# Optimization experiments

Measured on AMD Instinct MI355X. Metric: run time of the kernel, lower is better.

Reference implementation:

```python
import jax, jax.numpy as jnp
import numpy as np

B, C, H, W = 32, 512, 32, 32
D = C // 8

def setup_inputs() -> dict:
    key = jax.random.key(0)
    ks = jax.random.split(key, 5)
    return {
        "x": jax.random.normal(ks[0], (B, C, H, W), dtype=jnp.float32),
        "w1": jax.random.normal(ks[1], (D, C), dtype=jnp.float32) * (1.0 / np.sqrt(C)),
        "b1": jax.random.normal(ks[2], (D,), dtype=jnp.float32) * 0.01,
        "w2": jax.random.normal(ks[3], (C, C), dtype=jnp.float32) * (1.0 / np.sqrt(C)),
        "b2": jax.random.normal(ks[4], (C,), dtype=jnp.float32) * 0.01,
    }

def reference(x, w1, b1, w2, b2):
    b, c, h, w = x.shape
    n = h * w
    xf = x.reshape(b, c, n)                                   # [B,C,N]
    # 1x1 convs == channel-mixing GEMMs; conv1 is shared for q and k
    qk = jnp.einsum('bcn,dc->bdn', xf, w1) + b1[None, :, None]  # [B,D,N]
    v = jnp.einsum('bcn,oc->bon', xf, w2) + b2[None, :, None]   # [B,C,N]
    q = qk.transpose(0, 2, 1)                                 # [B,N,D]
    attn = jax.nn.softmax(jnp.einsum('bnd,bdm->bnm', q, qk), axis=-1)  # [B,N,N]
    out = jnp.einsum('bnm,bcm->bnc', attn, v)                 # [B,N,C]
    # Faithful quirk: original views [B,N,C] directly as [B,C,H,W] (no transpose)
    return x + out.reshape(b, c, h, w)
```

## Files before the change

### kernel.cpp

```cpp
#include <hip/hip_runtime.h>
#include <hip/hip_bf16.h>
#include <math.h>

#define B_ 32
#define C_ 512
#define N_ 1024
#define D_ 64
#define OPAD 640

typedef __attribute__((ext_vector_type(4))) float f32x4;
typedef __attribute__((ext_vector_type(4))) float float4v;
typedef __attribute__((ext_vector_type(8))) __bf16 bf16x8;

#define MFMA16(a, b, c) __builtin_amdgcn_mfma_f32_16x16x32_bf16((a), (b), (c), 0, 0, 0)

__device__ inline void load_lds16(const void* g, void* l) {
    __builtin_amdgcn_global_load_lds(
        (const __attribute__((address_space(1))) void*)g,
        (__attribute__((address_space(3))) void*)l, 16, 0, 0);
}

__global__ __launch_bounds__(256) void k_transpose_cast(
        const float* __restrict__ x,
        const float* __restrict__ w1, const float* __restrict__ w2,
        __hip_bfloat16* __restrict__ xT, __hip_bfloat16* __restrict__ Wbf) {
    __shared__ float tile[64][68];
    int b = blockIdx.z;
    int n0 = blockIdx.x * 64;
    int c0 = blockIdx.y * 64;
    int t = threadIdx.x;

    int lid = blockIdx.x + 16 * blockIdx.y + 128 * blockIdx.z;
    if (lid < 160) {
        int base = lid * 2048 + t * 8;
        int m = base >> 9, k = base & 511;
        alignas(16) __hip_bfloat16 wtmp[8];
        if (m < D_ + C_) {
            const float* s = (m < D_) ? w1 + (size_t)m * C_ + k
                                      : w2 + (size_t)(m - D_) * C_ + k;
            float4v a = *(const float4v*)s;
            float4v c = *(const float4v*)(s + 4);
            wtmp[0] = __float2bfloat16(a.x); wtmp[1] = __float2bfloat16(a.y);
            wtmp[2] = __float2bfloat16(a.z); wtmp[3] = __float2bfloat16(a.w);
            wtmp[4] = __float2bfloat16(c.x); wtmp[5] = __float2bfloat16(c.y);
            wtmp[6] = __float2bfloat16(c.z); wtmp[7] = __float2bfloat16(c.w);
        } else {
#pragma unroll
            for (int j = 0; j < 8; j++) wtmp[j] = __float2bfloat16(0.0f);
        }
        *(bf16x8*)(Wbf + base) = *(bf16x8*)wtmp;
    }

    const float* xb = x + (size_t)b * (C_ * N_);
#pragma unroll
    for (int i = 0; i < 4; i++) {
        int c = i * 16 + (t >> 4);
        int nc = (t & 15) * 4;
        *(float4v*)&tile[c][nc] =
            *(const float4v*)(xb + (size_t)(c0 + c) * N_ + n0 + nc);
    }
    __syncthreads();
    __hip_bfloat16* xTb = xT + (size_t)b * (N_ * C_);
#pragma unroll
    for (int i = 0; i < 2; i++) {
        int n = i * 32 + (t >> 3);
        int cs = (t & 7) * 8;
        alignas(16) __hip_bfloat16 tmp[8];
#pragma unroll
        for (int j = 0; j < 8; j++)
            tmp[j] = __float2bfloat16(tile[cs + j][n]);
        *(bf16x8*)(xTb + (size_t)(n0 + n) * C_ + c0 + cs) = *(bf16x8*)tmp;
    }
}

__global__ __launch_bounds__(256) void k_gemm_qkv(
        const __hip_bfloat16* __restrict__ Wbf,
        const __hip_bfloat16* __restrict__ xT,
        const float* __restrict__ b1, const float* __restrict__ b2,
        __hip_bfloat16* __restrict__ qkT, __hip_bfloat16* __restrict__ v) {
    __shared__ __hip_bfloat16 AB[2][2][128 * 64];
    __hip_bfloat16* epi = &AB[0][0][0];
    int b = blockIdx.x;
    int t = threadIdx.x;
    int wave = t >> 6, lane = t & 63, lr = lane & 15, quad = lane >> 4;
    int wm = wave >> 1, wn = wave & 1;
    int m_blk = blockIdx.z * 128;
    int n_blk = blockIdx.y * 128;
    const __hip_bfloat16* xTb = xT + (size_t)b * (N_ * C_);

#pragma unroll
    for (int i = 0; i < 4; i++) {
        int id = i * 256 + t;
        int r = id >> 3, cx = id & 7, gc = cx ^ (r & 7);
        load_lds16(Wbf + (size_t)(m_blk + r) * C_ + gc * 8, &AB[0][0][id * 8]);
        load_lds16(xTb + (size_t)(n_blk + r) * C_ + gc * 8, &AB[0][1][id * 8]);
    }
    __syncthreads();

    f32x4 acc[4][4] = {};
    for (int tt = 0; tt < 8; tt++) {
        const __hip_bfloat16* As = AB[tt & 1][0];
        const __hip_bfloat16* Bs = AB[tt & 1][1];
        if (tt < 7) {
            int kk = (tt + 1) * 64;
            __hip_bfloat16* An = AB[(tt + 1) & 1][0];
            __hip_bfloat16* Bn = AB[(tt + 1) & 1][1];
#pragma unroll
            for (int i = 0; i < 4; i++) {
                int id = i * 256 + t;
                int r = id >> 3, cx = id & 7, gc = cx ^ (r & 7);
                load_lds16(Wbf + (size_t)(m_blk + r) * C_ + kk + gc * 8, &An[id * 8]);
                load_lds16(xTb + (size_t)(n_blk + r) * C_ + kk + gc * 8, &Bn[id * 8]);
            }
        }
#pragma unroll
        for (int h = 0; h < 2; h++) {
            bf16x8 af[4], bfr[4];
#pragma unroll
            for (int i = 0; i < 4; i++) {
                int ra = wm * 64 + i * 16 + lr;
                int rb = wn * 64 + i * 16 + lr;
                int q = h * 4 + quad;
                af[i]  = *(const bf16x8*)&As[ra * 64 + (q ^ (lr & 7)) * 8];
                bfr[i] = *(const bf16x8*)&Bs[rb * 64 + (q ^ (lr & 7)) * 8];
            }
#pragma unroll
            for (int mt = 0; mt < 4; mt++)
#pragma unroll
                for (int nt = 0; nt < 4; nt++)
                    acc[mt][nt] = MFMA16(af[mt], bfr[nt], acc[mt][nt]);
        }
        __syncthreads();
    }

#pragma unroll
    for (int mt = 0; mt < 4; mt++) {
        int m_frag = m_blk + wm * 64 + mt * 16;
        if (m_frag >= D_ + C_) continue;
        int m0 = m_frag + quad * 4;
        if (m_frag < D_) {
#pragma unroll
            for (int nt = 0; nt < 4; nt++) {
                int n = n_blk + wn * 64 + nt * 16 + lr;
                alignas(8) __hip_bfloat16 tmp[4];
#pragma unroll
                for (int r = 0; r < 4; r++)
                    tmp[r] = __float2bfloat16(acc[mt][nt][r] + b1[m0 + r]);
                *reinterpret_cast<short4*>(qkT + ((size_t)b * N_ + n) * D_ + m0) =
                    *reinterpret_cast<short4*>(tmp);
            }
        } else {
#pragma unroll
            for (int nt = 0; nt < 4; nt++) {
#pragma unroll
                for (int r = 0; r < 4; r++) {
                    int c = m0 - D_ + r;
                    epi[(wave * 16 + quad * 4 + r) * 72 + nt * 16 + lr] =
                        __float2bfloat16(acc[mt][nt][r] + b2[c]);
                }
            }
            int cbase = m_frag - D_;
            int row = lane >> 2;
#pragma unroll
            for (int it = 0; it < 2; it++) {
                int col = it * 32 + (lane & 3) * 8;
                bf16x8 frag = *(const bf16x8*)&epi[(wave * 16 + row) * 72 + col];
                *(bf16x8*)(v + (size_t)(b * C_ + cbase + row) * N_
                             + n_blk + wn * 64 + col) = frag;
            }
        }
    }
}

__global__ __launch_bounds__(512, 2) void k_fused_attn(
        const __hip_bfloat16* __restrict__ qkT,
        const __hip_bfloat16* __restrict__ v,
        const float* __restrict__ x, float* __restrict__ out) {
    __shared__ char smem[155648];
    __hip_bfloat16* Ks  = (__hip_bfloat16*)smem;
    __hip_bfloat16* Vs0 = (__hip_bfloat16*)(smem + 8192);
    __hip_bfloat16* Vs1 = (__hip_bfloat16*)(smem + 73728);
    __hip_bfloat16* Ps  = (__hip_bfloat16*)(smem + 139264);
    float* Obuf = (float*)smem;
    float* Rs   = (float*)(smem + 66560);

    int b = blockIdx.x;
    int t = threadIdx.x;
    int wave = t >> 6, lane = t & 63, lr = lane & 15, quad = lane >> 4;
    int wm = wave >> 2, wn = wave & 3;
    int n_blk = blockIdx.y * 128;
    const __hip_bfloat16* qb = qkT + (size_t)b * (N_ * D_);
    const __hip_bfloat16* vb = v + (size_t)b * (C_ * N_);

    {
        int r = t >> 3, cxx = t & 7, gc = cxx ^ (r & 7);
        load_lds16(qb + (size_t)r * D_ + gc * 8, &Ks[t * 8]);
    }
#pragma unroll
    for (int i = 0; i < 8; i++) {
        int id = i * 512 + t;
        int r = id >> 3, cxx = id & 7, gc = cxx ^ (r & 7);
        load_lds16(vb + (size_t)r * N_ + gc * 8, &Vs0[id * 8]);
    }

    union bfu { bf16x8 v; __hip_bfloat16 h[8]; };
    bf16x8 bq[2];
    float shift;
    {
        int nq = n_blk + wave * 16 + lr;
        bq[0] = *(const bf16x8*)(qb + (size_t)nq * D_ + quad * 8);
        bq[1] = *(const bf16x8*)(qb + (size_t)nq * D_ + 32 + quad * 8);
        float sq = 0.f;
#pragma unroll
        for (int dh = 0; dh < 2; dh++) {
            bfu u; u.v = bq[dh];
#pragma unroll
            for (int j = 0; j < 8; j++) {
                float qv = __bfloat162float(u.h[j]);
                sq += qv * qv;
            }
        }
        sq += __shfl_xor(sq, 16);
        sq += __shfl_xor(sq, 32);
        shift = sq;
    }

    f32x4 acc[4][8] = {};
    float rsum = 0.f;

    __syncthreads();

    for (int tt = 0; tt < 16; ++tt) {
        int kk = tt * 64;
        __hip_bfloat16* Vcur = (tt & 1) ? Vs1 : Vs0;
        __hip_bfloat16* Vnxt = (tt & 1) ? Vs0 : Vs1;

        if (tt < 15) {
#pragma unroll
            for (int i = 0; i < 8; i++) {
                int id = i * 512 + t;
                int r = id >> 3, cxx = id & 7, gc = cxx ^ (r & 7);
                load_lds16(vb + (size_t)r * N_ + kk + 64 + gc * 8, &Vnxt[id * 8]);
            }
        }

#pragma unroll
        for (int mi = 0; mi < 4; mi++) {
            int m = mi * 16 + lr;
            bf16x8 ak0 = *(const bf16x8*)&Ks[m * 64 + ((quad) ^ (lr & 7)) * 8];
            bf16x8 ak1 = *(const bf16x8*)&Ks[m * 64 + ((4 + quad) ^ (lr & 7)) * 8];
            f32x4 s = {};
            s = MFMA16(ak0, bq[0], s);
            s = MFMA16(ak1, bq[1], s);
            alignas(8) __hip_bfloat16 tmp[4];
#pragma unroll
            for (int r = 0; r < 4; r++) {
                float e = __expf(s[r] - shift);
                rsum += e;
                tmp[r] = __float2bfloat16(e);
            }
            int n = wave * 16 + lr;
            int cx2 = mi * 2 + (quad >> 1);
            int slot = cx2 ^ (lr & 7);
            *(short4*)&Ps[n * 64 + slot * 8 + (quad & 1) * 4] = *(short4*)tmp;
        }

        asm volatile("s_waitcnt lgkmcnt(0)" ::: "memory");
        __builtin_amdgcn_s_barrier();
        __builtin_amdgcn_sched_barrier(0);

        if (tt < 15) {
            int r = t >> 3, cxx = t & 7, gc = cxx ^ (r & 7);
            load_lds16(qb + (size_t)(kk + 64 + r) * D_ + gc * 8, &Ks[t * 8]);
        }

#pragma unroll
        for (int h = 0; h < 2; h++) {
            bf16x8 af[4];
#pragma unroll
            for (int i = 0; i < 4; i++) {
                int ra = wm * 64 + i * 16 + lr;
                af[i] = *(const bf16x8*)&Ps[ra * 64 + ((h * 4 + quad) ^ (lr & 7)) * 8];
            }
#pragma unroll
            for (int g = 0; g < 2; g++) {
                bf16x8 bfr[4];
#pragma unroll
                for (int j = 0; j < 4; j++) {
                    int rb = wn * 128 + (g * 4 + j) * 16 + lr;
                    bfr[j] = *(const bf16x8*)&Vcur[rb * 64 + ((h * 4 + quad) ^ (lr & 7)) * 8];
                }
#pragma unroll
                for (int mt = 0; mt < 4; mt++)
#pragma unroll
                    for (int j = 0; j < 4; j++)
                        acc[mt][g * 4 + j] = MFMA16(af[mt], bfr[j], acc[mt][g * 4 + j]);
            }
        }
        __syncthreads();
    }

    rsum += __shfl_xor(rsum, 16);
    rsum += __shfl_xor(rsum, 32);
    if (quad == 0) Rs[wave * 16 + lr] = 1.0f / rsum;

    const float* xb = x + (size_t)b * (N_ * C_);
    float* ob = out + (size_t)b * (N_ * C_);
#pragma unroll
    for (int h = 0; h < 2; h++) {
#pragma unroll
        for (int g = 0; g < 2; g++) {
            __syncthreads();
            if (wm == h && (wn >> 1) == g) {
#pragma unroll
                for (int mt = 0; mt < 4; mt++)
#pragma unroll
                    for (int nt = 0; nt < 8; nt++)
#pragma unroll
                        for (int r = 0; r < 4; r++)
                            Obuf[(mt * 16 + quad * 4 + r) * 260
                                 + (wn & 1) * 128 + nt * 16 + lr] =
                                acc[mt][nt][r];
            }
            __syncthreads();
#pragma unroll
            for (int i = 0; i < 8; i++) {
                int id = i * 512 + t;
                int rl = id >> 6;
                int c4 = (id & 63) * 4;
                int n = n_blk + h * 64 + rl;
                float ri = Rs[h * 64 + rl];
                float4v o = *(const float4v*)&Obuf[rl * 260 + c4];
                size_t gidx = (size_t)n * C_ + g * 256 + c4;
                float4v xv = *(const float4v*)(xb + gidx);
                float4v res;
                res.x = xv.x + ri * o.x;
                res.y = xv.y + ri * o.y;
                res.z = xv.z + ri * o.z;
                res.w = xv.w + ri * o.w;
                *(float4v*)(ob + gidx) = res;
            }
        }
    }
}

extern "C" void kernel_launch(void* const* d_in, const int* in_sizes, int n_in,
                              void* d_out, int out_size, void* d_ws, size_t ws_size,
                              hipStream_t stream) {
    const float* x  = (const float*)d_in[0];
    const float* w1 = (const float*)d_in[1];
    const float* b1 = (const float*)d_in[2];
    const float* w2 = (const float*)d_in[3];
    const float* b2 = (const float*)d_in[4];
    float* out = (float*)d_out;

    char* ws = (char*)d_ws;
    size_t off = 0;
    __hip_bfloat16* Wbf = (__hip_bfloat16*)(ws + off); off += (size_t)OPAD * C_ * 2;
    __hip_bfloat16* xT  = (__hip_bfloat16*)(ws + off); off += (size_t)B_ * N_ * C_ * 2;
    __hip_bfloat16* qkT = (__hip_bfloat16*)(ws + off); off += (size_t)B_ * N_ * D_ * 2;
    __hip_bfloat16* v   = (__hip_bfloat16*)(ws + off); off += (size_t)B_ * C_ * N_ * 2;

    hipLaunchKernelGGL(k_transpose_cast, dim3(N_ / 64, C_ / 64, B_), dim3(256), 0, stream,
                       x, w1, w2, xT, Wbf);
    hipLaunchKernelGGL(k_gemm_qkv, dim3(B_, N_ / 128, OPAD / 128), dim3(256), 0, stream,
                       Wbf, xT, b1, b2, qkT, v);
    hipLaunchKernelGGL(k_fused_attn, dim3(B_, N_ / 128), dim3(512), 0, stream,
                       qkT, v, x, out);
}
```

Before: 203.5 us.

## Retile fused attention to 64-query by 256-channel blocks with 256 threads

```diff
diff --git a/kernel.cpp b/kernel.cpp
--- a/kernel.cpp
+++ b/kernel.cpp
@@ -172,35 +172,38 @@
     }
 }
 
-__global__ __launch_bounds__(512, 2) void k_fused_attn(
+__global__ __launch_bounds__(256, 2) void k_fused_attn(
         const __hip_bfloat16* __restrict__ qkT,
         const __hip_bfloat16* __restrict__ v,
         const float* __restrict__ x, float* __restrict__ out) {
-    __shared__ char smem[155648];
+    __shared__ char smem[81920];
     __hip_bfloat16* Ks  = (__hip_bfloat16*)smem;
-    __hip_bfloat16* Vs0 = (__hip_bfloat16*)(smem + 8192);
-    __hip_bfloat16* Vs1 = (__hip_bfloat16*)(smem + 73728);
-    __hip_bfloat16* Ps  = (__hip_bfloat16*)(smem + 139264);
+    __hip_bfloat16* Ps  = (__hip_bfloat16*)(smem + 8192);
+    __hip_bfloat16* Vs0 = (__hip_bfloat16*)(smem + 16384);
+    __hip_bfloat16* Vs1 = (__hip_bfloat16*)(smem + 49152);
     float* Obuf = (float*)smem;
-    float* Rs   = (float*)(smem + 66560);
+    float* Rs   = (float*)(smem + 73728);
 
     int b = blockIdx.x;
     int t = threadIdx.x;
     int wave = t >> 6, lane = t & 63, lr = lane & 15, quad = lane >> 4;
-    int wm = wave >> 2, wn = wave & 3;
-    int n_blk = blockIdx.y * 128;
+    int wn = wave;
+    int n_blk = blockIdx.y * 64;
+    int c_blk = blockIdx.z * 256;
     const __hip_bfloat16* qb = qkT + (size_t)b * (N_ * D_);
     const __hip_bfloat16* vb = v + (size_t)b * (C_ * N_);
 
-    {
-        int r = t >> 3, cxx = t & 7, gc = cxx ^ (r & 7);
-        load_lds16(qb + (size_t)r * D_ + gc * 8, &Ks[t * 8]);
+#pragma unroll
+    for (int i = 0; i < 2; i++) {
+        int id = i * 256 + t;
+        int r = id >> 3, cxx = id & 7, gc = cxx ^ (r & 7);
+        load_lds16(qb + (size_t)r * D_ + gc * 8, &Ks[id * 8]);
     }
 #pragma unroll
     for (int i = 0; i < 8; i++) {
-        int id = i * 512 + t;
+        int id = i * 256 + t;
         int r = id >> 3, cxx = id & 7, gc = cxx ^ (r & 7);
-        load_lds16(vb + (size_t)r * N_ + gc * 8, &Vs0[id * 8]);
+        load_lds16(vb + (size_t)(c_blk + r) * N_ + gc * 8, &Vs0[id * 8]);
     }
 
     union bfu { bf16x8 v; __hip_bfloat16 h[8]; };
@@ -225,7 +228,7 @@
         shift = sq;
     }
 
-    f32x4 acc[4][8] = {};
+    f32x4 acc[4][4] = {};
     float rsum = 0.f;
 
     __syncthreads();
@@ -238,9 +241,10 @@
         if (tt < 15) {
 #pragma unroll
             for (int i = 0; i < 8; i++) {
-                int id = i * 512 + t;
+                int id = i * 256 + t;
                 int r = id >> 3, cxx = id & 7, gc = cxx ^ (r & 7);
-                load_lds16(vb + (size_t)r * N_ + kk + 64 + gc * 8, &Vnxt[id * 8]);
+                load_lds16(vb + (size_t)(c_blk + r) * N_ + kk + 64 + gc * 8,
+                           &Vnxt[id * 8]);
             }
         }
 
@@ -270,32 +274,30 @@
         __builtin_amdgcn_sched_barrier(0);
 
         if (tt < 15) {
-            int r = t >> 3, cxx = t & 7, gc = cxx ^ (r & 7);
-            load_lds16(qb + (size_t)(kk + 64 + r) * D_ + gc * 8, &Ks[t * 8]);
+#pragma unroll
+            for (int i = 0; i < 2; i++) {
+                int id = i * 256 + t;
+                int r = id >> 3, cxx = id & 7, gc = cxx ^ (r & 7);
+                load_lds16(qb + (size_t)(kk + 64 + r) * D_ + gc * 8, &Ks[id * 8]);
+            }
         }
 
 #pragma unroll
         for (int h = 0; h < 2; h++) {
-            bf16x8 af[4];
+            bf16x8 af[4], bfr[4];
 #pragma unroll
             for (int i = 0; i < 4; i++) {
-                int ra = wm * 64 + i * 16 + lr;
-                af[i] = *(const bf16x8*)&Ps[ra * 64 + ((h * 4 + quad) ^ (lr & 7)) * 8];
-            }
-#pragma unroll
-            for (int g = 0; g < 2; g++) {
-                bf16x8 bfr[4];
-#pragma unroll
-                for (int j = 0; j < 4; j++) {
-                    int rb = wn * 128 + (g * 4 + j) * 16 + lr;
-                    bfr[j] = *(const bf16x8*)&Vcur[rb * 64 + ((h * 4 + quad) ^ (lr & 7)) * 8];
-                }
-#pragma unroll
-                for (int mt = 0; mt < 4; mt++)
-#pragma unroll
-                    for (int j = 0; j < 4; j++)
-                        acc[mt][g * 4 + j] = MFMA16(af[mt], bfr[j], acc[mt][g * 4 + j]);
-            }
+                int ra = i * 16 + lr;
+                int rb = wn * 64 + i * 16 + lr;
+                int q = h * 4 + quad;
+                af[i]  = *(const bf16x8*)&Ps[ra * 64 + (q ^ (lr & 7)) * 8];
+                bfr[i] = *(const bf16x8*)&Vcur[rb * 64 + (q ^ (lr & 7)) * 8];
+            }
+#pragma unroll
+            for (int mt = 0; mt < 4; mt++)
+#pragma unroll
+                for (int j = 0; j < 4; j++)
+                    acc[mt][j] = MFMA16(af[mt], bfr[j], acc[mt][j]);
         }
         __syncthreads();
     }
@@ -303,44 +305,36 @@
     rsum += __shfl_xor(rsum, 16);
     rsum += __shfl_xor(rsum, 32);
     if (quad == 0) Rs[wave * 16 + lr] = 1.0f / rsum;
+    __syncthreads();
+
+#pragma unroll
+    for (int mt = 0; mt < 4; mt++)
+#pragma unroll
+        for (int nt = 0; nt < 4; nt++)
+#pragma unroll
+            for (int r = 0; r < 4; r++)
+                Obuf[(mt * 16 + quad * 4 + r) * 260 + wn * 64 + nt * 16 + lr] =
+                    acc[mt][nt][r];
+    __syncthreads();
 
     const float* xb = x + (size_t)b * (N_ * C_);
     float* ob = out + (size_t)b * (N_ * C_);
 #pragma unroll
-    for (int h = 0; h < 2; h++) {
-#pragma unroll
-        for (int g = 0; g < 2; g++) {
-            __syncthreads();
-            if (wm == h && (wn >> 1) == g) {
-#pragma unroll
-                for (int mt = 0; mt < 4; mt++)
-#pragma unroll
-                    for (int nt = 0; nt < 8; nt++)
-#pragma unroll
-                        for (int r = 0; r < 4; r++)
-                            Obuf[(mt * 16 + quad * 4 + r) * 260
-                                 + (wn & 1) * 128 + nt * 16 + lr] =
-                                acc[mt][nt][r];
-            }
-            __syncthreads();
-#pragma unroll
-            for (int i = 0; i < 8; i++) {
-                int id = i * 512 + t;
-                int rl = id >> 6;
-                int c4 = (id & 63) * 4;
-                int n = n_blk + h * 64 + rl;
-                float ri = Rs[h * 64 + rl];
-                float4v o = *(const float4v*)&Obuf[rl * 260 + c4];
-                size_t gidx = (size_t)n * C_ + g * 256 + c4;
-                float4v xv = *(const float4v*)(xb + gidx);
-                float4v res;
-                res.x = xv.x + ri * o.x;
-                res.y = xv.y + ri * o.y;
-                res.z = xv.z + ri * o.z;
-                res.w = xv.w + ri * o.w;
-                *(float4v*)(ob + gidx) = res;
-            }
-        }
+    for (int i = 0; i < 16; i++) {
+        int id = i * 256 + t;
+        int rl = id >> 6;
+        int c4 = (id & 63) * 4;
+        int n = n_blk + rl;
+        float ri = Rs[rl];
+        float4v o = *(const float4v*)&Obuf[rl * 260 + c4];
+        size_t gidx = (size_t)n * C_ + c_blk + c4;
+        float4v xv = *(const float4v*)(xb + gidx);
+        float4v res;
+        res.x = xv.x + ri * o.x;
+        res.y = xv.y + ri * o.y;
+        res.z = xv.z + ri * o.z;
+        res.w = xv.w + ri * o.w;
+        *(float4v*)(ob + gidx) = res;
     }
 }
 
@@ -365,6 +359,6 @@
                        x, w1, w2, xT, Wbf);
     hipLaunchKernelGGL(k_gemm_qkv, dim3(B_, N_ / 128, OPAD / 128), dim3(256), 0, stream,
                        Wbf, xT, b1, b2, qkT, v);
-    hipLaunchKernelGGL(k_fused_attn, dim3(B_, N_ / 128), dim3(512), 0, stream,
+    hipLaunchKernelGGL(k_fused_attn, dim3(B_, N_ / 64, C_ / 256), dim3(256), 0, stream,
                        qkT, v, x, out);
 }
```

Result: slower. 214.5 us (+5.4%).
